# Kernel optimization log

Measured on AMD Instinct MI355X. Metric: run time of the kernel, lower is better.

The kernel has to match this reference:

```python
import jax, jax.numpy as jnp
import numpy as np

EPS = 1e-5

def layer_norm(x, w, b, eps=EPS):
    mu = jnp.mean(x, axis=-1, keepdims=True)
    var = jnp.mean(jnp.square(x - mu), axis=-1, keepdims=True)
    return (x - mu) * jax.lax.rsqrt(var + eps) * w + b

def setup_inputs() -> dict:
    key = jax.random.key(0)
    ks = jax.random.split(key, 8)
    B, N, D = 1, 512, 128
    x = jax.random.normal(ks[0], (B, N, N, D), dtype=jnp.float32)
    mask = jnp.ones((B, N, N), dtype=jnp.float32)
    # parameters (torch nn.Linear weight layout: [out, in], y = x @ W.T)
    scale = 1.0 / np.sqrt(D)
    return {
        "x": x,
        "mask": mask,
        "norm_in_w": jnp.ones((D,), jnp.float32),
        "norm_in_b": jnp.zeros((D,), jnp.float32),
        "p_in_w": jax.random.normal(ks[1], (2 * D, D), jnp.float32) * scale,
        "g_in_w": jax.random.normal(ks[2], (2 * D, D), jnp.float32) * scale,
        "norm_out_w": jnp.ones((D,), jnp.float32),
        "norm_out_b": jnp.zeros((D,), jnp.float32),
        "p_out_w": jax.random.normal(ks[3], (D, D), jnp.float32) * scale,
        "g_out_w": jax.random.normal(ks[4], (D, D), jnp.float32) * scale,
    }

def reference(x, mask, norm_in_w, norm_in_b, p_in_w, g_in_w,
              norm_out_w, norm_out_b, p_out_w, g_out_w):
    # x: (B, N, N, D); mask: (B, N, N)
    x_in = layer_norm(x, norm_in_w, norm_in_b)
    # gated projection to 2D channels, then mask
    h = (x_in @ p_in_w.T) * jax.nn.sigmoid(x_in @ g_in_w.T)  # (B,N,N,2D)
    h = h * mask[..., None]
    h = h.astype(jnp.float32)
    D = x.shape[-1]
    a, b = h[..., :D], h[..., D:]
    # outgoing triangle: contract over k per channel d
    t = jnp.einsum('bikd,bjkd->bijd', a, b)  # (B,N,N,D)
    out = (layer_norm(t, norm_out_w, norm_out_b) @ p_out_w.T) * jax.nn.sigmoid(x_in @ g_out_w.T)
    return out
```

## Files before the change

kernel.cpp:

```cpp
#include <hip/hip_runtime.h>

typedef unsigned short u16;
typedef _Float16 f16x8 __attribute__((ext_vector_type(8)));
typedef float f32x4 __attribute__((ext_vector_type(4)));

__device__ __forceinline__ u16 f2h(float f){
  _Float16 h = (_Float16)f; u16 u; __builtin_memcpy(&u, &h, 2); return u;
}
__device__ __forceinline__ float h2f(u16 u){
  _Float16 h; __builtin_memcpy(&h, &u, 2); return (float)h;
}
__device__ __forceinline__ unsigned pk2h(float a, float b){
  auto r = __builtin_amdgcn_cvt_pkrtz(a, b);
  unsigned u; __builtin_memcpy(&u, &r, 4); return u;
}
__device__ __forceinline__ float sigm(float x){ return 1.0f/(1.0f + __expf(-x)); }
__device__ __forceinline__ f32x4 zero4(){ f32x4 z; z[0]=0.f; z[1]=0.f; z[2]=0.f; z[3]=0.f; return z; }

#define SWZ8(row,k) ((k) ^ (((row)&7)<<3))
#define FRAG(n,kk,hi,col) ((((n)*4+(kk))*4+(hi))*16+(col))

__global__ void k_prep(const float* __restrict__ p_in, const float* __restrict__ g_in,
                       const float* __restrict__ g_out, const float* __restrict__ p_out,
                       u16* __restrict__ W1F, u16* __restrict__ WgoF, u16* __restrict__ WpoF){
  int t = blockIdx.x*256 + threadIdx.x;
  if (t < 65536){
    int c = t >> 13, u = t & 8191, f = u >> 3, e = u & 7;
    int col = f & 15, hi = (f>>4)&3, kk = (f>>6)&3, n = f>>8;
    int d = c*32 + (n>>1)*16 + col, k = kk*32 + hi*8 + e;
    W1F[t] = f2h((n&1) ? g_in[d*128+k] : p_in[d*128+k]);
  } else if (t < 81920){
    int u = t - 65536, f = u>>3, e = u&7;
    int col = f&15, hi=(f>>4)&3, kk=(f>>6)&3, n=f>>8;
    WgoF[u] = f2h(g_out[(n*16+col)*128 + kk*32+hi*8+e]);
  } else if (t < 98304){
    int u = t - 81920, f = u>>3, e = u&7;
    int col=f&15, hi=(f>>4)&3, kk=(f>>6)&3, n=f>>8;
    WpoF[u] = f2h(p_out[(n*16+col)*128 + kk*32+hi*8+e]);
  }
}

__global__ __launch_bounds__(256,2) void k_s1(
    const float* __restrict__ x, const float* __restrict__ mask,
    const float* __restrict__ nw, const float* __restrict__ nb,
    const u16* __restrict__ W1F,
    u16* __restrict__ a_t, u16* __restrict__ b_t, u16* __restrict__ x16f)
{
  __shared__ u16 xh_s[128*128];
  __shared__ float mask_s[128];

  const int tid = threadIdx.x, lane = tid & 63, w = tid >> 6;
  const int col = lane & 15, hi = lane >> 4;
  const int r0 = blockIdx.x * 128;

  if (tid < 128) mask_s[tid] = mask[r0 + tid];

  {
    const int g = lane >> 4, cl = lane & 15;
    float4 nwa = *(const float4*)(nw + cl*8);
    float4 nwb = *(const float4*)(nw + cl*8 + 4);
    float4 nba = *(const float4*)(nb + cl*8);
    float4 nbb = *(const float4*)(nb + cl*8 + 4);
    #pragma unroll
    for (int it = 0; it < 8; ++it){
      int row = w*32 + it*4 + g;
      const float* xr = x + (size_t)(r0+row)*128 + cl*8;
      float4 xa = *(const float4*)xr;
      float4 xb = *(const float4*)(xr + 4);
      float s = ((xa.x+xa.y)+(xa.z+xa.w)) + ((xb.x+xb.y)+(xb.z+xb.w));
      float q = xa.x*xa.x; q = fmaf(xa.y,xa.y,q); q = fmaf(xa.z,xa.z,q); q = fmaf(xa.w,xa.w,q);
      q = fmaf(xb.x,xb.x,q); q = fmaf(xb.y,xb.y,q); q = fmaf(xb.z,xb.z,q); q = fmaf(xb.w,xb.w,q);
      #pragma unroll
      for (int off = 1; off < 16; off <<= 1){ s += __shfl_xor(s, off); q += __shfl_xor(q, off); }
      float mu = s * 0.0078125f;
      float rs = rsqrtf(fmaxf(q*0.0078125f - mu*mu, 0.f) + 1e-5f);
      uint4 pv;
      pv.x = pk2h((xa.x-mu)*rs*nwa.x+nba.x, (xa.y-mu)*rs*nwa.y+nba.y);
      pv.y = pk2h((xa.z-mu)*rs*nwa.z+nba.z, (xa.w-mu)*rs*nwa.w+nba.w);
      pv.z = pk2h((xb.x-mu)*rs*nwb.x+nbb.x, (xb.y-mu)*rs*nwb.y+nbb.y);
      pv.w = pk2h((xb.z-mu)*rs*nwb.z+nbb.z, (xb.w-mu)*rs*nwb.w+nbb.w);
      *(uint4*)(&xh_s[row*128 + SWZ8(row, cl*8)]) = pv;
    }
  }
  __syncthreads();

  f16x8 af[2][4];
  #pragma unroll
  for (int m = 0; m < 2; ++m){
    #pragma unroll
    for (int kk = 0; kk < 4; ++kk){
      int row = w*32 + m*16 + col;
      af[m][kk] = *(const f16x8*)(&xh_s[row*128 + SWZ8(row, kk*32 + hi*8)]);
    }
  }
  float mk[2][4];
  #pragma unroll
  for (int m = 0; m < 2; ++m)
    #pragma unroll
    for (int j = 0; j < 4; ++j) mk[m][j] = mask_s[w*32 + m*16 + hi*4 + j];

  {
    u16* dst = x16f + (size_t)blockIdx.x*16384;
    #pragma unroll
    for (int m = 0; m < 2; ++m)
      #pragma unroll
      for (int kk = 0; kk < 4; ++kk)
        *(f16x8*)(dst + (size_t)FRAG(w*2+m, kk, hi, col)*8) = af[m][kk];
  }
  __syncthreads();

  for (int c = 0; c < 8; ++c){
    f32x4 acc[2][4];
    #pragma unroll
    for (int m = 0; m < 2; ++m)
      #pragma unroll
      for (int n = 0; n < 4; ++n) acc[m][n] = zero4();

    #pragma unroll
    for (int kk = 0; kk < 4; ++kk){
      f16x8 bf[4];
      #pragma unroll
      for (int n = 0; n < 4; ++n)
        bf[n] = *(const f16x8*)(W1F + c*8192 + (size_t)FRAG(n,kk,hi,col)*8);
      #pragma unroll
      for (int m = 0; m < 2; ++m)
        #pragma unroll
        for (int n = 0; n < 4; ++n)
          acc[m][n] = __builtin_amdgcn_mfma_f32_16x16x32_f16(af[m][kk], bf[n], acc[m][n], 0, 0, 0);
    }

    u16* hbuf = xh_s + (c & 1)*4096;
    #pragma unroll
    for (int m = 0; m < 2; ++m){
      #pragma unroll
      for (int t2 = 0; t2 < 2; ++t2){
        f32x4 pv = acc[m][2*t2], gv = acc[m][2*t2+1];
        int dl = t2*16 + col;
        int rb = w*32 + m*16 + hi*4;
        int ad = dl*128 + (rb ^ ((dl & 15) << 3));
        float h0 = pv[0]*sigm(gv[0])*mk[m][0];
        float h1 = pv[1]*sigm(gv[1])*mk[m][1];
        float h2 = pv[2]*sigm(gv[2])*mk[m][2];
        float h3 = pv[3]*sigm(gv[3])*mk[m][3];
        uint2 uv; uv.x = pk2h(h0, h1); uv.y = pk2h(h2, h3);
        *(uint2*)(&hbuf[ad]) = uv;
      }
    }
    __syncthreads();
    {
      int dl = tid >> 3, seg = (tid & 7)*16;
      int dg = c*32 + dl;
      u16* dst = (dg < 128 ? a_t + (size_t)dg*262144 : b_t + (size_t)(dg-128)*262144) + r0;
      int sw = (dl & 15) << 3;
      uint4 v0 = *(const uint4*)(&hbuf[dl*128 + (seg ^ sw)]);
      uint4 v1 = *(const uint4*)(&hbuf[dl*128 + ((seg + 8) ^ sw)]);
      *(uint4*)(dst + seg)     = v0;
      *(uint4*)(dst + seg + 8) = v1;
    }
  }
}

__global__ __launch_bounds__(256,4) void k_s2(
    const u16* __restrict__ a_t, const u16* __restrict__ b_t, u16* __restrict__ t_dm)
{
  __shared__ u16 AB_s[2][2][4096];

  const int tid = threadIdx.x, lane = tid & 63, w = tid >> 6;
  const int col = lane & 15, hi = lane >> 4;

  int bid = blockIdx.x + (blockIdx.y << 4);
  int sw = (bid & 7)*256 + (bid >> 3);
  const int d = sw >> 4;
  const int tile = sw & 15;
  const int ti = (tile >> 2) * 128, tj = (tile & 3) * 128;
  const u16* Ab = a_t + (size_t)d * 262144;
  const u16* Bb = b_t + (size_t)d * 262144;
  const int wr = (w >> 1) * 64, wc = (w & 1) * 64;

  f32x4 acc[4][4];
  #pragma unroll
  for (int m=0;m<4;m++){
    #pragma unroll
    for (int n=0;n<4;n++) acc[m][n] = zero4();
  }

  const int srow = lane >> 2;
  const int scol = (lane & 3) * 8;

  auto STAGE = [&](int buf, int k0){
    #pragma unroll
    for (int j = 0; j < 2; ++j){
      int chunk = w*2 + j;
      int row = chunk*16 + srow;
      int e = scol ^ ((((row >> 1) & 3)) << 3);
      const unsigned int* gpA = (const unsigned int*)(Ab + (size_t)(ti + row)*512 + k0 + e);
      unsigned int* lpA = (unsigned int*)(&AB_s[buf][0][chunk*512]);
      __builtin_amdgcn_global_load_lds((const __attribute__((address_space(1))) unsigned int*)gpA,
                                       (__attribute__((address_space(3))) unsigned int*)lpA, 16, 0, 0);
      const unsigned int* gpB = (const unsigned int*)(Bb + (size_t)(tj + row)*512 + k0 + e);
      unsigned int* lpB = (unsigned int*)(&AB_s[buf][1][chunk*512]);
      __builtin_amdgcn_global_load_lds((const __attribute__((address_space(1))) unsigned int*)gpB,
                                       (__attribute__((address_space(3))) unsigned int*)lpB, 16, 0, 0);
    }
  };

  STAGE(0, 0);
  int cur = 0;
  for (int k0 = 0; k0 < 512; k0 += 32){
    __syncthreads();
    if (k0 + 32 < 512) STAGE(cur ^ 1, k0 + 32);
    f16x8 af[4], bfv[4];
    #pragma unroll
    for (int m=0;m<4;m++){
      int row = wr + m*16 + col;
      af[m] = *(const f16x8*)(&AB_s[cur][0][row*32 + (hi*8 ^ ((((row>>1)&3))<<3))]);
    }
    #pragma unroll
    for (int n=0;n<4;n++){
      int row = wc + n*16 + col;
      bfv[n] = *(const f16x8*)(&AB_s[cur][1][row*32 + (hi*8 ^ ((((row>>1)&3))<<3))]);
    }
    #pragma unroll
    for (int m=0;m<4;m++){
      #pragma unroll
      for (int n=0;n<4;n++)
        acc[m][n] = __builtin_amdgcn_mfma_f32_16x16x32_f16(af[m], bfv[n], acc[m][n], 0, 0, 0);
    }
    cur ^= 1;
  }

  u16* C_s = &AB_s[0][0][0];
  __syncthreads();
  u16* dst0 = t_dm + (size_t)d*262144 + (size_t)ti*512 + tj;
  #pragma unroll
  for (int h = 0; h < 2; ++h){
    if ((w >> 1) == h){
      #pragma unroll
      for (int m=0;m<4;m++){
        #pragma unroll
        for (int n=0;n<4;n++){
          #pragma unroll
          for (int j=0;j<4;j++){
            int row = m*16 + hi*4 + j, cl = wc + n*16 + col;
            C_s[row*136 + cl] = f2h(acc[m][n][j]);
          }
        }
      }
    }
    __syncthreads();
    #pragma unroll
    for (int s=0;s<4;s++){
      int gi = s*256 + tid;
      int row = gi >> 4, seg = (gi & 15) * 8;
      *(uint4*)(dst0 + (size_t)(h*64 + row)*512 + seg) = *(const uint4*)(&C_s[row*136 + seg]);
    }
    if (h == 0) __syncthreads();
  }
}

__global__ __launch_bounds__(256,1) void k_s3(
    const u16* __restrict__ t_dm, const u16* __restrict__ x16f,
    const u16* __restrict__ WgoF, const u16* __restrict__ WpoF,
    const float* __restrict__ nw, const float* __restrict__ nb,
    float* __restrict__ out)
{
  __shared__ u16 t_s[128*128];

  const int tid = threadIdx.x, lane = tid & 63, w = tid >> 6;
  const int col = lane & 15, hi = lane >> 4;
  const size_t rbase = (size_t)blockIdx.x * 128;

  const int dblk = tid >> 4, jblk = tid & 15;
  const u16* tsrc = t_dm + (size_t)(dblk*8)*262144 + rbase + jblk*8;
  uint4 rv[8];
  #pragma unroll
  for (int r=0;r<8;r++) rv[r] = *(const uint4*)(tsrc + (size_t)r*262144);

  f16x8 af[2][4];
  {
    const u16* base = x16f + (size_t)blockIdx.x*16384;
    #pragma unroll
    for (int m=0;m<2;m++)
      #pragma unroll
      for (int kk=0;kk<4;kk++)
        af[m][kk] = *(const f16x8*)(base + (size_t)FRAG(w*2+m, kk, hi, col)*8);
  }

  {
    const unsigned* pr = (const unsigned*)rv;
    #pragma unroll
    for (int jj=0;jj<8;jj++){
      int j = (jj + jblk) & 7;
      unsigned sel = (j&1) ? 0x07060302u : 0x05040100u;
      int dw = j >> 1;
      uint4 ov;
      ov.x = __builtin_amdgcn_perm(pr[4+dw],  pr[0+dw],  sel);
      ov.y = __builtin_amdgcn_perm(pr[12+dw], pr[8+dw],  sel);
      ov.z = __builtin_amdgcn_perm(pr[20+dw], pr[16+dw], sel);
      ov.w = __builtin_amdgcn_perm(pr[28+dw], pr[24+dw], sel);
      int row = jblk*8 + j;
      *(uint4*)(&t_s[row*128 + SWZ8(row, dblk*8)]) = ov;
    }
  }

  unsigned gt[2][8][2];
  {
    f32x4 gacc[2][8];
    #pragma unroll
    for (int m=0;m<2;m++)
      #pragma unroll
      for (int n=0;n<8;n++) gacc[m][n] = zero4();
    #pragma unroll
    for (int kk=0;kk<4;kk++){
      #pragma unroll
      for (int n=0;n<8;n++){
        f16x8 bv = *(const f16x8*)(WgoF + (size_t)FRAG(n,kk,hi,col)*8);
        #pragma unroll
        for (int m=0;m<2;m++)
          gacc[m][n] = __builtin_amdgcn_mfma_f32_16x16x32_f16(af[m][kk], bv, gacc[m][n], 0, 0, 0);
      }
    }
    #pragma unroll
    for (int m=0;m<2;m++)
      #pragma unroll
      for (int n=0;n<8;n++){
        gt[m][n][0] = pk2h(sigm(gacc[m][n][0]), sigm(gacc[m][n][1]));
        gt[m][n][1] = pk2h(sigm(gacc[m][n][2]), sigm(gacc[m][n][3]));
      }
  }
  __syncthreads();

  {
    int j = tid >> 1, dh = (tid & 1) * 64;
    float s = 0.f, q = 0.f;
    #pragma unroll
    for (int sc=0;sc<8;sc++){
      uint4 v = *(const uint4*)(&t_s[j*128 + SWZ8(j, dh + sc*8)]);
      const u16* ev = (const u16*)&v;
      #pragma unroll
      for (int u=0;u<8;u++){ float f = h2f(ev[u]); s += f; q = fmaf(f,f,q); }
    }
    s += __shfl_xor(s, 1); q += __shfl_xor(q, 1);
    float mu = s * 0.0078125f;
    float rs = rsqrtf(fmaxf(q*0.0078125f - mu*mu, 0.f) + 1e-5f);
    #pragma unroll
    for (int sc=0;sc<8;sc++){
      int db = dh + sc*8;
      u16* p = &t_s[j*128 + SWZ8(j, db)];
      uint4 v = *(uint4*)p;
      u16* ev = (u16*)&v;
      float4 w0 = *(const float4*)(nw + db);
      float4 w1 = *(const float4*)(nw + db + 4);
      float4 b0 = *(const float4*)(nb + db);
      float4 b1 = *(const float4*)(nb + db + 4);
      float wv[8] = {w0.x,w0.y,w0.z,w0.w,w1.x,w1.y,w1.z,w1.w};
      float bv[8] = {b0.x,b0.y,b0.z,b0.w,b1.x,b1.y,b1.z,b1.w};
      #pragma unroll
      for (int u=0;u<8;u++){
        float f = (h2f(ev[u]) - mu)*rs*wv[u] + bv[u];
        ev[u] = f2h(f);
      }
      *(uint4*)p = v;
    }
  }
  __syncthreads();

  f32x4 acc[2][8];
  #pragma unroll
  for (int m=0;m<2;m++){
    #pragma unroll
    for (int n=0;n<8;n++) acc[m][n] = zero4();
  }
  #pragma unroll
  for (int kk=0;kk<4;kk++){
    f16x8 a2[2];
    #pragma unroll
    for (int m=0;m<2;m++){
      int row = w*32 + m*16 + col;
      a2[m] = *(const f16x8*)(&t_s[row*128 + SWZ8(row, kk*32 + hi*8)]);
    }
    #pragma unroll
    for (int n=0;n<8;n++){
      f16x8 bv = *(const f16x8*)(WpoF + (size_t)FRAG(n,kk,hi,col)*8);
      #pragma unroll
      for (int m=0;m<2;m++)
        acc[m][n] = __builtin_amdgcn_mfma_f32_16x16x32_f16(a2[m], bv, acc[m][n], 0, 0, 0);
    }
  }
  __syncthreads();

  #pragma unroll
  for (int m=0;m<2;m++){
    #pragma unroll
    for (int n=0;n<8;n++){
      #pragma unroll
      for (int j=0;j<4;j++){
        int row = w*32 + m*16 + hi*4 + j, cl = n*16 + col;
        float g = h2f((u16)(gt[m][n][j>>1] >> ((j&1)*16)));
        t_s[row*128 + SWZ8(row, cl)] = f2h(acc[m][n][j] * g);
      }
    }
  }
  __syncthreads();

  {
    #pragma unroll
    for (int s=0;s<16;s++){
      int idx = s*256 + tid;
      int row = idx >> 5, c4 = (idx & 31) << 2;
      const u16* p = &t_s[row*128 + SWZ8(row, c4)];
      uint2 cv = *(const uint2*)p;
      const u16* ce = (const u16*)&cv;
      float4 o;
      o.x = h2f(ce[0]); o.y = h2f(ce[1]); o.z = h2f(ce[2]); o.w = h2f(ce[3]);
      *(float4*)(out + (rbase + row)*128 + c4) = o;
    }
  }
}

extern "C" void kernel_launch(void* const* d_in, const int* in_sizes, int n_in,
                              void* d_out, int out_size, void* d_ws, size_t ws_size,
                              hipStream_t stream){
  const float* x    = (const float*)d_in[0];
  const float* mask = (const float*)d_in[1];
  const float* niw  = (const float*)d_in[2];
  const float* nib  = (const float*)d_in[3];
  const float* piw  = (const float*)d_in[4];
  const float* giw  = (const float*)d_in[5];
  const float* now  = (const float*)d_in[6];
  const float* nob  = (const float*)d_in[7];
  const float* pow_ = (const float*)d_in[8];
  const float* gow  = (const float*)d_in[9];
  float* out = (float*)d_out;

  char* ws = (char*)d_ws;
  u16* a_t  = (u16*)(ws);
  u16* b_t  = (u16*)(ws + (size_t)67108864);
  u16* t_dm = (u16*)(ws + (size_t)134217728);
  u16* x16f = (u16*)(ws + (size_t)201326592);
  u16* W1F  = (u16*)(ws + (size_t)268435456);
  u16* WgoF = W1F + 65536;
  u16* WpoF = WgoF + 16384;

  k_prep<<<384, 256, 0, stream>>>(piw, giw, gow, pow_, W1F, WgoF, WpoF);
  k_s1<<<2048, 256, 0, stream>>>(x, mask, niw, nib, W1F, a_t, b_t, x16f);
  k_s2<<<dim3(16,128), 256, 0, stream>>>(a_t, b_t, t_dm);
  k_s3<<<2048, 256, 0, stream>>>(t_dm, x16f, WgoF, WpoF, now, nob, out);
}
```

Before: 286.8 us.

## Split stage-1 into layernorm and per-chunk projection kernels for more parallelism

Stage 1 is split into a layernorm kernel that writes normalized fp16 fragments to global memory and a projection kernel. The projection kernel launches one block per (row block, channel chunk) instead of looping over 8 chunks. The aim is more blocks in flight and no serial chunk loop with its barriers. In exchange the normalized activations are re-read from global memory 8 times and there is an extra kernel launch.

```diff
diff --git a/kernel.cpp b/kernel.cpp
--- a/kernel.cpp
+++ b/kernel.cpp
@@ -40,20 +40,16 @@
   }
 }
 
-__global__ __launch_bounds__(256,2) void k_s1(
-    const float* __restrict__ x, const float* __restrict__ mask,
+__global__ __launch_bounds__(256,2) void k_ln(
+    const float* __restrict__ x,
     const float* __restrict__ nw, const float* __restrict__ nb,
-    const u16* __restrict__ W1F,
-    u16* __restrict__ a_t, u16* __restrict__ b_t, u16* __restrict__ x16f)
+    u16* __restrict__ x16f)
 {
   __shared__ u16 xh_s[128*128];
-  __shared__ float mask_s[128];
 
   const int tid = threadIdx.x, lane = tid & 63, w = tid >> 6;
   const int col = lane & 15, hi = lane >> 4;
   const int r0 = blockIdx.x * 128;
-
-  if (tid < 128) mask_s[tid] = mask[r0 + tid];
 
   {
     const int g = lane >> 4, cl = lane & 15;
@@ -84,79 +80,92 @@
   }
   __syncthreads();
 
-  f16x8 af[2][4];
+  u16* dst = x16f + (size_t)blockIdx.x*16384;
   #pragma unroll
   for (int m = 0; m < 2; ++m){
     #pragma unroll
     for (int kk = 0; kk < 4; ++kk){
       int row = w*32 + m*16 + col;
-      af[m][kk] = *(const f16x8*)(&xh_s[row*128 + SWZ8(row, kk*32 + hi*8)]);
-    }
+      f16x8 v = *(const f16x8*)(&xh_s[row*128 + SWZ8(row, kk*32 + hi*8)]);
+      *(f16x8*)(dst + (size_t)FRAG(w*2+m, kk, hi, col)*8) = v;
+    }
+  }
+}
+
+__global__ __launch_bounds__(256,2) void k_proj(
+    const float* __restrict__ mask, const u16* __restrict__ W1F,
+    const u16* __restrict__ x16f,
+    u16* __restrict__ a_t, u16* __restrict__ b_t)
+{
+  __shared__ u16 hbuf[32*128];
+
+  const int tid = threadIdx.x, lane = tid & 63, w = tid >> 6;
+  const int col = lane & 15, hi = lane >> 4;
+  const int bid = blockIdx.x;
+  const int rb = bid >> 3, c = bid & 7;
+  const int r0 = rb * 128;
+
+  f16x8 af[2][4];
+  {
+    const u16* base = x16f + (size_t)rb*16384;
+    #pragma unroll
+    for (int m=0;m<2;m++)
+      #pragma unroll
+      for (int kk=0;kk<4;kk++)
+        af[m][kk] = *(const f16x8*)(base + (size_t)FRAG(w*2+m, kk, hi, col)*8);
   }
   float mk[2][4];
   #pragma unroll
   for (int m = 0; m < 2; ++m)
     #pragma unroll
-    for (int j = 0; j < 4; ++j) mk[m][j] = mask_s[w*32 + m*16 + hi*4 + j];
-
-  {
-    u16* dst = x16f + (size_t)blockIdx.x*16384;
+    for (int j = 0; j < 4; ++j)
+      mk[m][j] = mask[r0 + w*32 + m*16 + hi*4 + j];
+
+  f32x4 acc[2][4];
+  #pragma unroll
+  for (int m = 0; m < 2; ++m)
+    #pragma unroll
+    for (int n = 0; n < 4; ++n) acc[m][n] = zero4();
+
+  #pragma unroll
+  for (int kk = 0; kk < 4; ++kk){
+    f16x8 bf[4];
+    #pragma unroll
+    for (int n = 0; n < 4; ++n)
+      bf[n] = *(const f16x8*)(W1F + c*8192 + (size_t)FRAG(n,kk,hi,col)*8);
     #pragma unroll
     for (int m = 0; m < 2; ++m)
       #pragma unroll
-      for (int kk = 0; kk < 4; ++kk)
-        *(f16x8*)(dst + (size_t)FRAG(w*2+m, kk, hi, col)*8) = af[m][kk];
-  }
-  __syncthreads();
-
-  for (int c = 0; c < 8; ++c){
-    f32x4 acc[2][4];
-    #pragma unroll
-    for (int m = 0; m < 2; ++m)
-      #pragma unroll
-      for (int n = 0; n < 4; ++n) acc[m][n] = zero4();
-
-    #pragma unroll
-    for (int kk = 0; kk < 4; ++kk){
-      f16x8 bf[4];
-      #pragma unroll
       for (int n = 0; n < 4; ++n)
-        bf[n] = *(const f16x8*)(W1F + c*8192 + (size_t)FRAG(n,kk,hi,col)*8);
-      #pragma unroll
-      for (int m = 0; m < 2; ++m)
-        #pragma unroll
-        for (int n = 0; n < 4; ++n)
-          acc[m][n] = __builtin_amdgcn_mfma_f32_16x16x32_f16(af[m][kk], bf[n], acc[m][n], 0, 0, 0);
-    }
-
-    u16* hbuf = xh_s + (c & 1)*4096;
-    #pragma unroll
-    for (int m = 0; m < 2; ++m){
-      #pragma unroll
-      for (int t2 = 0; t2 < 2; ++t2){
-        f32x4 pv = acc[m][2*t2], gv = acc[m][2*t2+1];
-        int dl = t2*16 + col;
-        int rb = w*32 + m*16 + hi*4;
-        int ad = dl*128 + (rb ^ ((dl & 15) << 3));
-        float h0 = pv[0]*sigm(gv[0])*mk[m][0];
-        float h1 = pv[1]*sigm(gv[1])*mk[m][1];
-        float h2 = pv[2]*sigm(gv[2])*mk[m][2];
-        float h3 = pv[3]*sigm(gv[3])*mk[m][3];
-        uint2 uv; uv.x = pk2h(h0, h1); uv.y = pk2h(h2, h3);
-        *(uint2*)(&hbuf[ad]) = uv;
-      }
-    }
-    __syncthreads();
-    {
-      int dl = tid >> 3, seg = (tid & 7)*16;
-      int dg = c*32 + dl;
-      u16* dst = (dg < 128 ? a_t + (size_t)dg*262144 : b_t + (size_t)(dg-128)*262144) + r0;
-      int sw = (dl & 15) << 3;
-      uint4 v0 = *(const uint4*)(&hbuf[dl*128 + (seg ^ sw)]);
-      uint4 v1 = *(const uint4*)(&hbuf[dl*128 + ((seg + 8) ^ sw)]);
-      *(uint4*)(dst + seg)     = v0;
-      *(uint4*)(dst + seg + 8) = v1;
-    }
+        acc[m][n] = __builtin_amdgcn_mfma_f32_16x16x32_f16(af[m][kk], bf[n], acc[m][n], 0, 0, 0);
+  }
+
+  #pragma unroll
+  for (int m = 0; m < 2; ++m){
+    #pragma unroll
+    for (int t2 = 0; t2 < 2; ++t2){
+      f32x4 pv = acc[m][2*t2], gv = acc[m][2*t2+1];
+      int dl = t2*16 + col;
+      int rbw = w*32 + m*16 + hi*4;
+      int ad = dl*128 + (rbw ^ ((dl & 15) << 3));
+      float h0 = pv[0]*sigm(gv[0])*mk[m][0];
+      float h1 = pv[1]*sigm(gv[1])*mk[m][1];
+      float h2 = pv[2]*sigm(gv[2])*mk[m][2];
+      float h3 = pv[3]*sigm(gv[3])*mk[m][3];
+      uint2 uv; uv.x = pk2h(h0, h1); uv.y = pk2h(h2, h3);
+      *(uint2*)(&hbuf[ad]) = uv;
+    }
+  }
+  __syncthreads();
+  {
+    int dl = tid >> 3, seg = (tid & 7)*16;
+    int dg = c*32 + dl;
+    u16* dst = (dg < 128 ? a_t + (size_t)dg*262144 : b_t + (size_t)(dg-128)*262144) + r0;
+    int sw = (dl & 15) << 3;
+    uint4 v0 = *(const uint4*)(&hbuf[dl*128 + (seg ^ sw)]);
+    uint4 v1 = *(const uint4*)(&hbuf[dl*128 + ((seg + 8) ^ sw)]);
+    *(uint4*)(dst + seg)     = v0;
+    *(uint4*)(dst + seg + 8) = v1;
   }
 }
 
@@ -443,7 +452,8 @@
   u16* WpoF = WgoF + 16384;
 
   k_prep<<<384, 256, 0, stream>>>(piw, giw, gow, pow_, W1F, WgoF, WpoF);
-  k_s1<<<2048, 256, 0, stream>>>(x, mask, niw, nib, W1F, a_t, b_t, x16f);
-  k_s2<<<dim3(16,128), 256, 0, stream>>>(a_t, b_t, t_dm);
-  k_s3<<<2048, 256, 0, stream>>>(t_dm, x16f, WgoF, WpoF, now, nob, out);
-}
+  k_ln  <<<2048, 256, 0, stream>>>(x, niw, nib, x16f);
+  k_proj<<<16384, 256, 0, stream>>>(mask, W1F, x16f, a_t, b_t);
+  k_s2  <<<dim3(16,128), 256, 0, stream>>>(a_t, b_t, t_dm);
+  k_s3  <<<2048, 256, 0, stream>>>(t_dm, x16f, WgoF, WpoF, now, nob, out);
+}
```

Result: slower. 322.6 us (+12.5%).

## Compute output gate sigmoid in stage 1 and store gate instead of x_in

Applied to the files above, without the earlier changes.

The output gate sigmoid(x_in @ g_out_w.T) moves from k_s3 into k_s1, where the normalized x fragments are already in registers. k_s1 writes the fp16 gate through shared memory instead of the fp16 x_in fragments, and k_s3 reads the gate and applies it during the final fp32 store. Global traffic stays about the same, since both buffers are 128 fp16 values per row. The gain comes from lower register pressure and less MFMA work in k_s3, which runs at occupancy 1, while k_s1 gains extra MFMAs and two more barrier rounds.

```diff
diff --git a/kernel.cpp b/kernel.cpp
--- a/kernel.cpp
+++ b/kernel.cpp
@@ -43,8 +43,8 @@
 __global__ __launch_bounds__(256,2) void k_s1(
     const float* __restrict__ x, const float* __restrict__ mask,
     const float* __restrict__ nw, const float* __restrict__ nb,
-    const u16* __restrict__ W1F,
-    u16* __restrict__ a_t, u16* __restrict__ b_t, u16* __restrict__ x16f)
+    const u16* __restrict__ W1F, const u16* __restrict__ WgoF,
+    u16* __restrict__ a_t, u16* __restrict__ b_t, u16* __restrict__ gate)
 {
   __shared__ u16 xh_s[128*128];
   __shared__ float mask_s[128];
@@ -98,15 +98,6 @@
   for (int m = 0; m < 2; ++m)
     #pragma unroll
     for (int j = 0; j < 4; ++j) mk[m][j] = mask_s[w*32 + m*16 + hi*4 + j];
-
-  {
-    u16* dst = x16f + (size_t)blockIdx.x*16384;
-    #pragma unroll
-    for (int m = 0; m < 2; ++m)
-      #pragma unroll
-      for (int kk = 0; kk < 4; ++kk)
-        *(f16x8*)(dst + (size_t)FRAG(w*2+m, kk, hi, col)*8) = af[m][kk];
-  }
   __syncthreads();
 
   for (int c = 0; c < 8; ++c){
@@ -158,6 +149,47 @@
       *(uint4*)(dst + seg + 8) = v1;
     }
   }
+  __syncthreads();
+
+  u16* gbuf = xh_s;
+  #pragma unroll
+  for (int gc = 0; gc < 2; ++gc){
+    f32x4 acc[2][4];
+    #pragma unroll
+    for (int m = 0; m < 2; ++m)
+      #pragma unroll
+      for (int n = 0; n < 4; ++n) acc[m][n] = zero4();
+    #pragma unroll
+    for (int kk = 0; kk < 4; ++kk){
+      f16x8 bf[4];
+      #pragma unroll
+      for (int n = 0; n < 4; ++n)
+        bf[n] = *(const f16x8*)(WgoF + (size_t)FRAG(gc*4+n, kk, hi, col)*8);
+      #pragma unroll
+      for (int m = 0; m < 2; ++m)
+        #pragma unroll
+        for (int n = 0; n < 4; ++n)
+          acc[m][n] = __builtin_amdgcn_mfma_f32_16x16x32_f16(af[m][kk], bf[n], acc[m][n], 0, 0, 0);
+    }
+    #pragma unroll
+    for (int m = 0; m < 2; ++m)
+      #pragma unroll
+      for (int n = 0; n < 4; ++n)
+        #pragma unroll
+        for (int j = 0; j < 4; ++j){
+          int row = w*32 + m*16 + hi*4 + j;
+          gbuf[row*68 + n*16 + col] = f2h(sigm(acc[m][n][j]));
+        }
+    __syncthreads();
+    {
+      int row = tid >> 1, base = (tid & 1)*32;
+      u16* dst = gate + (size_t)(r0+row)*128 + gc*64 + base;
+      #pragma unroll
+      for (int i2 = 0; i2 < 4; ++i2)
+        *(uint4*)(dst + i2*8) = *(const uint4*)(&gbuf[row*68 + base + i2*8]);
+    }
+    __syncthreads();
+  }
 }
 
 __global__ __launch_bounds__(256,4) void k_s2(
@@ -259,8 +291,8 @@
 }
 
 __global__ __launch_bounds__(256,1) void k_s3(
-    const u16* __restrict__ t_dm, const u16* __restrict__ x16f,
-    const u16* __restrict__ WgoF, const u16* __restrict__ WpoF,
+    const u16* __restrict__ t_dm, const u16* __restrict__ gate,
+    const u16* __restrict__ WpoF,
     const float* __restrict__ nw, const float* __restrict__ nb,
     float* __restrict__ out)
 {
@@ -275,16 +307,6 @@
   uint4 rv[8];
   #pragma unroll
   for (int r=0;r<8;r++) rv[r] = *(const uint4*)(tsrc + (size_t)r*262144);
-
-  f16x8 af[2][4];
-  {
-    const u16* base = x16f + (size_t)blockIdx.x*16384;
-    #pragma unroll
-    for (int m=0;m<2;m++)
-      #pragma unroll
-      for (int kk=0;kk<4;kk++)
-        af[m][kk] = *(const f16x8*)(base + (size_t)FRAG(w*2+m, kk, hi, col)*8);
-  }
 
   {
     const unsigned* pr = (const unsigned*)rv;
@@ -302,32 +324,6 @@
       *(uint4*)(&t_s[row*128 + SWZ8(row, dblk*8)]) = ov;
     }
   }
-
-  unsigned gt[2][8][2];
-  {
-    f32x4 gacc[2][8];
-    #pragma unroll
-    for (int m=0;m<2;m++)
-      #pragma unroll
-      for (int n=0;n<8;n++) gacc[m][n] = zero4();
-    #pragma unroll
-    for (int kk=0;kk<4;kk++){
-      #pragma unroll
-      for (int n=0;n<8;n++){
-        f16x8 bv = *(const f16x8*)(WgoF + (size_t)FRAG(n,kk,hi,col)*8);
-        #pragma unroll
-        for (int m=0;m<2;m++)
-          gacc[m][n] = __builtin_amdgcn_mfma_f32_16x16x32_f16(af[m][kk], bv, gacc[m][n], 0, 0, 0);
-      }
-    }
-    #pragma unroll
-    for (int m=0;m<2;m++)
-      #pragma unroll
-      for (int n=0;n<8;n++){
-        gt[m][n][0] = pk2h(sigm(gacc[m][n][0]), sigm(gacc[m][n][1]));
-        gt[m][n][1] = pk2h(sigm(gacc[m][n][2]), sigm(gacc[m][n][3]));
-      }
-  }
   __syncthreads();
 
   {
@@ -396,8 +392,7 @@
       #pragma unroll
       for (int j=0;j<4;j++){
         int row = w*32 + m*16 + hi*4 + j, cl = n*16 + col;
-        float g = h2f((u16)(gt[m][n][j>>1] >> ((j&1)*16)));
-        t_s[row*128 + SWZ8(row, cl)] = f2h(acc[m][n][j] * g);
+        t_s[row*128 + SWZ8(row, cl)] = f2h(acc[m][n][j]);
       }
     }
   }
@@ -410,9 +405,14 @@
       int row = idx >> 5, c4 = (idx & 31) << 2;
       const u16* p = &t_s[row*128 + SWZ8(row, c4)];
       uint2 cv = *(const uint2*)p;
+      uint2 gv = *(const uint2*)(gate + (rbase + row)*128 + c4);
       const u16* ce = (const u16*)&cv;
+      const u16* ge = (const u16*)&gv;
       float4 o;
-      o.x = h2f(ce[0]); o.y = h2f(ce[1]); o.z = h2f(ce[2]); o.w = h2f(ce[3]);
+      o.x = h2f(ce[0])*h2f(ge[0]);
+      o.y = h2f(ce[1])*h2f(ge[1]);
+      o.z = h2f(ce[2])*h2f(ge[2]);
+      o.w = h2f(ce[3])*h2f(ge[3]);
       *(float4*)(out + (rbase + row)*128 + c4) = o;
     }
   }
@@ -437,13 +437,13 @@
   u16* a_t  = (u16*)(ws);
   u16* b_t  = (u16*)(ws + (size_t)67108864);
   u16* t_dm = (u16*)(ws + (size_t)134217728);
-  u16* x16f = (u16*)(ws + (size_t)201326592);
+  u16* gate = (u16*)(ws + (size_t)201326592);
   u16* W1F  = (u16*)(ws + (size_t)268435456);
   u16* WgoF = W1F + 65536;
   u16* WpoF = WgoF + 16384;
 
   k_prep<<<384, 256, 0, stream>>>(piw, giw, gow, pow_, W1F, WgoF, WpoF);
-  k_s1<<<2048, 256, 0, stream>>>(x, mask, niw, nib, W1F, a_t, b_t, x16f);
+  k_s1<<<2048, 256, 0, stream>>>(x, mask, niw, nib, W1F, WgoF, a_t, b_t, gate);
   k_s2<<<dim3(16,128), 256, 0, stream>>>(a_t, b_t, t_dm);
-  k_s3<<<2048, 256, 0, stream>>>(t_dm, x16f, WgoF, WpoF, now, nob, out);
-}
+  k_s3<<<2048, 256, 0, stream>>>(t_dm, gate, WpoF, now, nob, out);
+}
```

New measurement: 329.2 us. 1.15x slower.
